# Optimization experiments

Hardware: AMD Instinct MI355X
Metric: run time of the kernel (lower is better)

Reference implementation:

```python
import jax, jax.numpy as jnp
import numpy as np

N_HEAD = 16
N_EMBD = 1024
B, T = 4, 2048


def setup_inputs() -> dict:
    key = jax.random.key(0)
    ks = jax.random.split(key, 5)
    s_in = 1.0 / np.sqrt(N_EMBD)
    return {
        "x": jax.random.normal(ks[0], (B, T, N_EMBD), dtype=jnp.float32),
        "W_qkv": jax.random.normal(ks[1], (N_EMBD, 3 * N_EMBD), dtype=jnp.float32) * s_in,
        "b_qkv": jnp.zeros((3 * N_EMBD,), dtype=jnp.float32),
        "W_proj": jax.random.normal(ks[2], (N_EMBD, N_EMBD), dtype=jnp.float32) * s_in,
        "b_proj": jnp.zeros((N_EMBD,), dtype=jnp.float32),
    }


def reference(x, W_qkv, b_qkv, W_proj, b_proj):
    Bb, Tt, C = x.shape
    H = N_HEAD
    hd = C // H  # head dim
    qkv = x @ W_qkv + b_qkv                      # [B,T,3C]
    q, k, v = jnp.split(qkv, 3, axis=-1)
    # [B,H,T,hd]
    q = q.reshape(Bb, Tt, H, hd).transpose(0, 2, 1, 3)
    k = k.reshape(Bb, Tt, H, hd).transpose(0, 2, 1, 3)
    v = v.reshape(Bb, Tt, H, hd).transpose(0, 2, 1, 3)
    scale = 1.0 / np.sqrt(hd).astype(np.float32)
    att = jnp.einsum("bhqd,bhkd->bhqk", q, k) * scale
    causal = jnp.tril(jnp.ones((Tt, Tt), dtype=bool))
    att = jnp.where(causal, att, jnp.float32(-jnp.inf))
    att = jax.nn.softmax(att, axis=-1)
    y = jnp.einsum("bhqk,bhkd->bhqd", att, v)    # [B,H,T,hd]
    y = y.transpose(0, 2, 1, 3).reshape(Bb, Tt, C)
    return y @ W_proj + b_proj
```

## Files before the change

kernel.cpp:

```cpp
#include <hip/hip_runtime.h>
#include <hip/hip_bf16.h>
#include <math.h>

typedef unsigned short u16;
typedef _Float16 f16_t;
typedef f16_t f16x8 __attribute__((ext_vector_type(8)));
typedef float f32x4 __attribute__((ext_vector_type(4)));

#define N_HEADC 16
#define C_EMBD  1024
#define B_SZ    4
#define T_SEQ   2048
#define HD      64
#define M_TOT   (B_SZ * T_SEQ)

#define BM 128
#define BN 256
#define BK 32
#define NT (C_EMBD / BK)
#define A_T (BM * BK)
#define B_T (BN * BK)

#define SWZ_CHUNK(l) ((((l) & 3) ^ (((l) >> 3) & 3)) * 8)

__device__ __forceinline__ u16 f2h(float f) {
    f16_t h = (f16_t)f;
    return __builtin_bit_cast(u16, h);
}
__device__ __forceinline__ unsigned pkf16(float a, float b) {
    unsigned lo = f2h(a), hi = f2h(b);
    return lo | (hi << 16);
}
__device__ __forceinline__ float fexp2(float x) {
#if __has_builtin(__builtin_amdgcn_exp2f)
    return __builtin_amdgcn_exp2f(x);
#else
    return exp2f(x);
#endif
}
__device__ __forceinline__ void gl_lds16(const u16* g, u16* l) {
    __builtin_amdgcn_global_load_lds(
        (const __attribute__((address_space(1))) unsigned int*)g,
        (__attribute__((address_space(3))) unsigned int*)l,
        16, 0, 0);
}

__global__ __launch_bounds__(256) void prep(const float* __restrict__ x,
                                            const float* __restrict__ Wqkv,
                                            const float* __restrict__ Wproj,
                                            u16* __restrict__ xh,
                                            u16* __restrict__ WqkvT,
                                            u16* __restrict__ WprojT) {
    __shared__ float tile[32][33];
    int bid = blockIdx.x, tid = threadIdx.x;
    if (bid < 8192) {
        int i = bid * 1024 + tid * 4;
        float4 v = *(const float4*)(x + i);
        ushort4 o;
        o.x = f2h(v.x); o.y = f2h(v.y); o.z = f2h(v.z); o.w = f2h(v.w);
        *(ushort4*)(xh + i) = o;
        return;
    }
    const float* in; u16* outp; int N, bx, by;
    if (bid < 8192 + 3072) {
        int b2 = bid - 8192; bx = b2 % 96; by = b2 / 96;
        in = Wqkv; outp = WqkvT; N = 3 * C_EMBD;
    } else {
        int b2 = bid - 11264; bx = b2 % 32; by = b2 / 32;
        in = Wproj; outp = WprojT; N = C_EMBD;
    }
    int tx = tid & 31, ty = tid >> 5;
    int n0 = bx * 32, k0 = by * 32;
    for (int i = ty; i < 32; i += 8)
        tile[i][tx] = in[(size_t)(k0 + i) * N + n0 + tx];
    __syncthreads();
    for (int i = ty; i < 32; i += 8)
        outp[(size_t)(n0 + i) * C_EMBD + k0 + tx] = f2h(tile[tx][i]);
}

__global__ __launch_bounds__(512) void gemm_qkv(const u16* __restrict__ A,
                                                const u16* __restrict__ BT,
                                                const float* __restrict__ bias,
                                                u16* __restrict__ qQ,
                                                u16* __restrict__ qK,
                                                u16* __restrict__ qVt) {
    __shared__ __align__(16) u16 smem[2 * A_T + 2 * B_T];
    u16* sA = smem;
    u16* sB = smem + 2 * A_T;
    int m0 = blockIdx.y * BM;
    int n0 = blockIdx.x * BN;
    int tid = threadIdx.x;
    int w = tid >> 6, lane = tid & 63;
    int wm = w >> 2, wn = w & 3;
    int quad = lane >> 4, rl = lane & 15;
    int srow = lane >> 2, sko = SWZ_CHUNK(lane);
    int kx = (rl >> 1) & 3;
    int qx = (quad ^ kx) * 8;

    f32x4 acc[4][4];
    #pragma unroll
    for (int i = 0; i < 4; ++i)
        #pragma unroll
        for (int j = 0; j < 4; ++j)
            acc[i][j] = f32x4{0.f, 0.f, 0.f, 0.f};

    const u16* gA  = A  + (size_t)(m0 + w * 16 + srow) * C_EMBD + sko;
    const u16* gB0 = BT + (size_t)(n0 + w * 16 + srow) * C_EMBD + sko;
    const u16* gB1 = gB0 + (size_t)128 * C_EMBD;

    gl_lds16(gA,  sA + w * 512);
    gl_lds16(gB0, sB + w * 512);
    gl_lds16(gB1, sB + 128 * BK + w * 512);
    gA += BK; gB0 += BK; gB1 += BK;

    for (int t = 0; t < NT; ++t) {
        asm volatile("s_waitcnt vmcnt(0)" ::: "memory");
        asm volatile("s_barrier" ::: "memory");
        const u16* pA = sA + (t & 1) * A_T + (wm * 64) * BK;
        const u16* pB = sB + (t & 1) * B_T + (wn * 64) * BK;
        f16x8 af[4], bfr[4];
        #pragma unroll
        for (int i = 0; i < 4; ++i)
            af[i] = *(const f16x8*)&pA[(i * 16 + rl) * BK + qx];
        bfr[0] = *(const f16x8*)&pB[(0 * 16 + rl) * BK + qx];
        bfr[1] = *(const f16x8*)&pB[(1 * 16 + rl) * BK + qx];
        if (t + 1 < NT) {
            int ns = (t + 1) & 1;
            gl_lds16(gA,  sA + ns * A_T + w * 512);
            gl_lds16(gB0, sB + ns * B_T + w * 512);
        }
        asm volatile("s_barrier" ::: "memory");
        __builtin_amdgcn_s_setprio(1);
        #pragma unroll
        for (int j = 0; j < 2; ++j)
            #pragma unroll
            for (int i = 0; i < 4; ++i)
                acc[i][j] = __builtin_amdgcn_mfma_f32_16x16x32_f16(
                    af[i], bfr[j], acc[i][j], 0, 0, 0);
        __builtin_amdgcn_s_setprio(0);
        asm volatile("s_barrier" ::: "memory");
        bfr[2] = *(const f16x8*)&pB[(2 * 16 + rl) * BK + qx];
        bfr[3] = *(const f16x8*)&pB[(3 * 16 + rl) * BK + qx];
        if (t + 1 < NT) {
            gl_lds16(gB1, sB + ((t + 1) & 1) * B_T + 128 * BK + w * 512);
            gA += BK; gB0 += BK; gB1 += BK;
        }
        asm volatile("s_barrier" ::: "memory");
        __builtin_amdgcn_s_setprio(1);
        #pragma unroll
        for (int j = 2; j < 4; ++j)
            #pragma unroll
            for (int i = 0; i < 4; ++i)
                acc[i][j] = __builtin_amdgcn_mfma_f32_16x16x32_f16(
                    af[i], bfr[j], acc[i][j], 0, 0, 0);
        __builtin_amdgcn_s_setprio(0);
    }

    __syncthreads();

    const float QSC = 0.18033688011112042f;
    int p = n0 >> 10;
    if (p < 2) {
        u16* ep = smem;
        u16* dst = p == 0 ? qQ : qK;
        float sc = p == 0 ? QSC : 1.0f;
        int hbase = (n0 & 1023) >> 6;
        #pragma unroll
        for (int c = 0; c < 4; ++c) {
            if (c) __syncthreads();
            if (wn == c) {
                #pragma unroll
                for (int j = 0; j < 4; ++j) {
                    float bv = bias[n0 + c * 64 + j * 16 + rl];
                    int col = (j * 16 + rl) ^ ((quad >> 1) << 4);
                    #pragma unroll
                    for (int i = 0; i < 4; ++i) {
                        int row = wm * 64 + i * 16 + quad * 4;
                        #pragma unroll
                        for (int r = 0; r < 4; ++r)
                            ep[(row + r) * 72 + col] = f2h((acc[i][j][r] + bv) * sc);
                    }
                }
            }
            __syncthreads();
            size_t rowbase = ((size_t)(m0 >> 11) * N_HEADC + hbase + c) * T_SEQ
                           + (m0 & 2047);
            #pragma unroll
            for (int s = 0; s < 2; ++s) {
                int task = s * 512 + tid;
                int row = task >> 3, seg = task & 7;
                int colr = (seg * 8) ^ (((row >> 3) & 1) << 4);
                *(uint4*)&dst[(rowbase + row) * HD + seg * 8] =
                    *(const uint4*)&ep[row * 72 + colr];
            }
        }
    } else {
        u16 (*tr)[136] = (u16 (*)[136])smem;
        int bb = m0 >> 11, t0g = m0 & 2047;
        #pragma unroll
        for (int c = 0; c < 4; ++c) {
            if (c) __syncthreads();
            if (wn == c) {
                #pragma unroll
                for (int j = 0; j < 4; ++j) {
                    int rowr = j * 16 + rl;
                    float bv = bias[n0 + c * 64 + rowr];
                    #pragma unroll
                    for (int i = 0; i < 4; ++i) {
                        int mm = wm * 64 + i * 16 + quad * 4;
                        *(unsigned*)&tr[rowr][mm]     = pkf16(acc[i][j][0] + bv, acc[i][j][1] + bv);
                        *(unsigned*)&tr[rowr][mm + 2] = pkf16(acc[i][j][2] + bv, acc[i][j][3] + bv);
                    }
                }
            }
            __syncthreads();
            #pragma unroll
            for (int s = 0; s < 2; ++s) {
                int task = s * 512 + tid;
                int nn = task >> 4, seg = task & 15;
                int ch = (n0 & 1023) + c * 64 + nn;
                int h = ch >> 6, d = ch & 63;
                size_t di = (((size_t)bb * N_HEADC + h) * HD + d) * T_SEQ + t0g + seg * 8;
                *(uint4*)&qVt[di] = *(const uint4*)&tr[nn][seg * 8];
            }
        }
    }
}

__global__ __launch_bounds__(512) void gemm_proj(const u16* __restrict__ A,
                                                 const u16* __restrict__ BT,
                                                 const float* __restrict__ bias,
                                                 float* __restrict__ out) {
    __shared__ __align__(16) u16 smem[3 * A_T + 3 * B_T];
    u16* sA = smem;
    u16* sB = smem + 3 * A_T;
    int m0 = blockIdx.y * BM;
    int n0 = blockIdx.x * BN;
    int tid = threadIdx.x;
    int w = tid >> 6, lane = tid & 63;
    int wm = w >> 2, wn = w & 3;
    int quad = lane >> 4, rl = lane & 15;
    int srow = lane >> 2, sko = SWZ_CHUNK(lane);
    int kx = (rl >> 1) & 3;
    int qx = (quad ^ kx) * 8;

    f32x4 acc[4][4];
    #pragma unroll
    for (int i = 0; i < 4; ++i)
        #pragma unroll
        for (int j = 0; j < 4; ++j)
            acc[i][j] = f32x4{0.f, 0.f, 0.f, 0.f};

    const u16* gA  = A  + (size_t)(m0 + w * 16 + srow) * C_EMBD + sko;
    const u16* gB0 = BT + (size_t)(n0 + w * 16 + srow) * C_EMBD + sko;
    const u16* gB1 = gB0 + (size_t)128 * C_EMBD;
    gl_lds16(gA,       sA + w * 512);
    gl_lds16(gB0,      sB + w * 512);
    gl_lds16(gB1,      sB + 128 * BK + w * 512);
    gl_lds16(gA + BK,  sA + A_T + w * 512);
    gl_lds16(gB0 + BK, sB + B_T + w * 512);
    gl_lds16(gB1 + BK, sB + B_T + 128 * BK + w * 512);
    gA += 2 * BK; gB0 += 2 * BK; gB1 += 2 * BK;
    int bufR = 0, bufS = 2;
    for (int t = 0; t < NT; ++t) {
        if (t == NT - 1) asm volatile("s_waitcnt vmcnt(0)" ::: "memory");
        else             asm volatile("s_waitcnt vmcnt(3)" ::: "memory");
        asm volatile("s_barrier" ::: "memory");
        const u16* pA = sA + bufR * A_T + (wm * 64) * BK;
        const u16* pB = sB + bufR * B_T + (wn * 64) * BK;
        f16x8 af[4], bfr[4];
        #pragma unroll
        for (int i = 0; i < 4; ++i)
            af[i] = *(const f16x8*)&pA[(i * 16 + rl) * BK + qx];
        bfr[0] = *(const f16x8*)&pB[(0 * 16 + rl) * BK + qx];
        bfr[1] = *(const f16x8*)&pB[(1 * 16 + rl) * BK + qx];
        if (t + 2 < NT) {
            gl_lds16(gA,  sA + bufS * A_T + w * 512);
            gl_lds16(gB0, sB + bufS * B_T + w * 512);
        }
        asm volatile("s_barrier" ::: "memory");
        __builtin_amdgcn_s_setprio(1);
        #pragma unroll
        for (int j = 0; j < 2; ++j)
            #pragma unroll
            for (int i = 0; i < 4; ++i)
                acc[i][j] = __builtin_amdgcn_mfma_f32_16x16x32_f16(
                    af[i], bfr[j], acc[i][j], 0, 0, 0);
        __builtin_amdgcn_s_setprio(0);
        asm volatile("s_barrier" ::: "memory");
        bfr[2] = *(const f16x8*)&pB[(2 * 16 + rl) * BK + qx];
        bfr[3] = *(const f16x8*)&pB[(3 * 16 + rl) * BK + qx];
        if (t + 2 < NT) {
            gl_lds16(gB1, sB + bufS * B_T + 128 * BK + w * 512);
            gA += BK; gB0 += BK; gB1 += BK;
        }
        asm volatile("s_barrier" ::: "memory");
        __builtin_amdgcn_s_setprio(1);
        #pragma unroll
        for (int j = 2; j < 4; ++j)
            #pragma unroll
            for (int i = 0; i < 4; ++i)
                acc[i][j] = __builtin_amdgcn_mfma_f32_16x16x32_f16(
                    af[i], bfr[j], acc[i][j], 0, 0, 0);
        __builtin_amdgcn_s_setprio(0);
        bufR = bufR == 2 ? 0 : bufR + 1;
        bufS = bufS == 2 ? 0 : bufS + 1;
    }

    #pragma unroll
    for (int i = 0; i < 4; ++i) {
        int mbase = m0 + wm * 64 + i * 16 + quad * 4;
        #pragma unroll
        for (int j = 0; j < 4; ++j) {
            int n = n0 + wn * 64 + j * 16 + rl;
            float bv = bias[n];
            #pragma unroll
            for (int r = 0; r < 4; ++r)
                out[(size_t)(mbase + r) * C_EMBD + n] = acc[i][j][r] + bv;
        }
    }
}

__global__ __launch_bounds__(512) void attn_mfma(const u16* __restrict__ Qg,
                                                 const u16* __restrict__ Kg,
                                                 const u16* __restrict__ Vtg,
                                                 u16* __restrict__ yh) {
    int bid = blockIdx.x;
    int a  = bid >> 6;
    int g  = bid & 63;
    int j  = a < 4 ? a : 11 - a;
    int h = g & 15, b = g >> 4;
    const size_t hs = (size_t)T_SEQ * HD;
    const u16* Qp  = Qg  + ((size_t)b * N_HEADC + h) * hs;
    const u16* Kp  = Kg  + ((size_t)b * N_HEADC + h) * hs;
    const u16* Vtp = Vtg + ((size_t)b * N_HEADC + h) * hs;

    __shared__ __align__(16) u16 sK[2][2][64][32];
    __shared__ __align__(16) u16 sVt[2][2][64][32];
    __shared__ __align__(16) u16 sP[8][32][72];

    int tid = threadIdx.x;
    int lane = tid & 63, w = tid >> 6;
    int quad = lane >> 4, rl = lane & 15;
    int kx = (rl >> 1) & 3;
    int qx = (quad ^ kx) * 8;
    u16* sPw = &sP[w][0][0];
    int srow = lane >> 2;
    int sch = SWZ_CHUNK(lane);
    const f32x4 mneg = {-4.f, -4.f, -4.f, -4.f};

    int qt  = (w < 4) ? (15 - j) : j;
    int q0w = qt * 128 + (w & 3) * 32;
    int nkt = 2 * (15 - j) + 2;

    const u16* gp[2];
    u16* ld0[2]; u16* ld1[2];
    int gstep;
    if (w < 4) {
        gstep = 64 * HD;
        int half = (w >> 1) & 1, rbase = (w & 1) * 32;
        #pragma unroll
        for (int c = 0; c < 2; ++c) {
            int r = rbase + c * 16;
            gp[c]  = Kp + (size_t)(r + srow) * HD + half * 32 + sch;
            ld0[c] = &sK[0][half][r][0];
            ld1[c] = &sK[1][half][r][0];
        }
    } else {
        gstep = 64;
        int v = w - 4;
        int half = (v >> 1) & 1, rbase = (v & 1) * 32;
        #pragma unroll
        for (int c = 0; c < 2; ++c) {
            int r = rbase + c * 16;
            gp[c]  = Vtp + (size_t)(r + srow) * T_SEQ + half * 32 + sch;
            ld0[c] = &sVt[0][half][r][0];
            ld1[c] = &sVt[1][half][r][0];
        }
    }

    f16x8 qf[2][2];
    #pragma unroll
    for (int nt = 0; nt < 2; ++nt)
        #pragma unroll
        for (int ks = 0; ks < 2; ++ks)
            qf[nt][ks] = *(const f16x8*)&Qp[(size_t)(q0w + nt * 16 + rl) * HD + ks * 32 + quad * 8];

    f32x4 O[2][4];
    #pragma unroll
    for (int mi = 0; mi < 2; ++mi)
        #pragma unroll
        for (int nd = 0; nd < 4; ++nd)
            O[mi][nd] = f32x4{0.f, 0.f, 0.f, 0.f};
    float l_[2] = {0.f, 0.f};

    gl_lds16(gp[0], ld0[0]);
    gl_lds16(gp[1], ld0[1]);

    for (int kt = 0; kt < nkt; ++kt) {
        __syncthreads();
        int buf = kt & 1;
        int k0 = kt * 64;
        if (kt + 1 < nkt) {
            u16* const* ldn = ((kt + 1) & 1) ? ld1 : ld0;
            #pragma unroll
            for (int c = 0; c < 2; ++c) {
                gp[c] += gstep;
                gl_lds16(gp[c], ldn[c]);
            }
        }
        if (k0 > q0w + 31) continue;

        f32x4 st[4][2];
        #pragma unroll
        for (int mt = 0; mt < 4; ++mt) {
            f16x8 ak0 = *(const f16x8*)&sK[buf][0][mt * 16 + rl][qx];
            f16x8 ak1 = *(const f16x8*)&sK[buf][1][mt * 16 + rl][qx];
            #pragma unroll
            for (int nt = 0; nt < 2; ++nt) {
                f32x4 t = __builtin_amdgcn_mfma_f32_16x16x32_f16(ak0, qf[nt][0], mneg, 0, 0, 0);
                st[mt][nt] = __builtin_amdgcn_mfma_f32_16x16x32_f16(ak1, qf[nt][1], t, 0, 0, 0);
            }
        }

        if (k0 + 63 > q0w) {
            #pragma unroll
            for (int mt = 0; mt < 4; ++mt)
                #pragma unroll
                for (int nt = 0; nt < 2; ++nt)
                    #pragma unroll
                    for (int r = 0; r < 4; ++r) {
                        int kpos = k0 + mt * 16 + quad * 4 + r;
                        int q = q0w + nt * 16 + rl;
                        if (kpos > q) st[mt][nt][r] = -INFINITY;
                    }
        }

        #pragma unroll
        for (int nt = 0; nt < 2; ++nt) {
            float lsum = 0.f;
            #pragma unroll
            for (int mt = 0; mt < 4; ++mt) {
                float p0 = fexp2(st[mt][nt][0]);
                float p1 = fexp2(st[mt][nt][1]);
                float p2 = fexp2(st[mt][nt][2]);
                float p3 = fexp2(st[mt][nt][3]);
                lsum += (p0 + p1) + (p2 + p3);
                *(uint2*)&sPw[(nt * 16 + rl) * 72 + mt * 16 + quad * 4] =
                    make_uint2(pkf16(p0, p1), pkf16(p2, p3));
            }
            l_[nt] += lsum;
        }

        #pragma unroll
        for (int ks = 0; ks < 2; ++ks) {
            f16x8 ap0 = *(const f16x8*)&sPw[(0 * 16 + rl) * 72 + ks * 32 + quad * 8];
            f16x8 ap1 = *(const f16x8*)&sPw[(1 * 16 + rl) * 72 + ks * 32 + quad * 8];
            #pragma unroll
            for (int nd = 0; nd < 4; ++nd) {
                f16x8 bv = *(const f16x8*)&sVt[buf][ks][nd * 16 + rl][qx];
                O[0][nd] = __builtin_amdgcn_mfma_f32_16x16x32_f16(ap0, bv, O[0][nd], 0, 0, 0);
                O[1][nd] = __builtin_amdgcn_mfma_f32_16x16x32_f16(ap1, bv, O[1][nd], 0, 0, 0);
            }
        }
    }

    #pragma unroll
    for (int nt = 0; nt < 2; ++nt) {
        l_[nt] += __shfl_xor(l_[nt], 16);
        l_[nt] += __shfl_xor(l_[nt], 32);
    }
    float linv[2] = {1.f / l_[0], 1.f / l_[1]};
    int idxq = quad * 4;
    #pragma unroll
    for (int mi = 0; mi < 2; ++mi)
        #pragma unroll
        for (int r = 0; r < 4; ++r) {
            float li = __shfl(linv[mi], idxq + r);
            int qg = q0w + mi * 16 + quad * 4 + r;
            size_t base = ((size_t)b * T_SEQ + qg) * C_EMBD + h * HD;
            #pragma unroll
            for (int nd = 0; nd < 4; ++nd)
                yh[base + nd * 16 + rl] = f2h(O[mi][nd][r] * li);
        }
}

extern "C" void kernel_launch(void* const* d_in, const int* in_sizes, int n_in,
                              void* d_out, int out_size, void* d_ws, size_t ws_size,
                              hipStream_t stream) {
    const float* x     = (const float*)d_in[0];
    const float* Wqkv  = (const float*)d_in[1];
    const float* bqkv  = (const float*)d_in[2];
    const float* Wproj = (const float*)d_in[3];
    const float* bproj = (const float*)d_in[4];
    float* out = (float*)d_out;

    char* ws = (char*)d_ws;
    u16* xh     = (u16*)(ws);
    u16* WqkvT  = (u16*)(ws + (size_t)16 * 1024 * 1024);
    u16* WprojT = (u16*)(ws + (size_t)22 * 1024 * 1024);
    u16* qQ     = (u16*)(ws + (size_t)24 * 1024 * 1024);
    u16* qK     = (u16*)(ws + (size_t)40 * 1024 * 1024);
    u16* qVt    = (u16*)(ws + (size_t)56 * 1024 * 1024);
    u16* yh     = (u16*)(ws + (size_t)72 * 1024 * 1024);

    prep<<<dim3(12288), dim3(256), 0, stream>>>(x, Wqkv, Wproj, xh, WqkvT, WprojT);
    gemm_qkv<<<dim3(3 * C_EMBD / BN, M_TOT / BM), dim3(512), 0, stream>>>(
        xh, WqkvT, bqkv, qQ, qK, qVt);
    attn_mfma<<<dim3(512), dim3(512), 0, stream>>>(
        qQ, qK, qVt, yh);
    gemm_proj<<<dim3(C_EMBD / BN, M_TOT / BM), dim3(512), 0, stream>>>(
        yh, WprojT, bproj, out);
}
```

Measured before the change: 237.3 us.

## Use 4-wave QKV GEMM with triple buffering and rework attention query tiling

The QKV GEMM drops to 256 threads, so each wave now computes a 128x64 tile. It switches from double to triple-buffered LDS with a partial vmcnt wait, so global loads overlap compute. The epilogue is now per-wave in private LDS regions, which removes the block-wide barriers between column chunks. The attention kernel changes its block-to-query-tile mapping from paired heavy/light 128-row tiles to single 256-row tiles ordered largest first. That trades causal load balancing within a block for simpler scheduling, and the larger per-wave accumulators raise register pressure.

```diff
diff --git a/kernel.cpp b/kernel.cpp
--- a/kernel.cpp
+++ b/kernel.cpp
@@ -20,6 +20,7 @@
 #define NT (C_EMBD / BK)
 #define A_T (BM * BK)
 #define B_T (BN * BK)
+#define SMEM_U16 (3 * A_T + 3 * B_T)
 
 #define SWZ_CHUNK(l) ((((l) & 3) ^ (((l) >> 3) & 3)) * 8)
 
@@ -78,151 +79,153 @@
         outp[(size_t)(n0 + i) * C_EMBD + k0 + tx] = f2h(tile[tx][i]);
 }
 
-__global__ __launch_bounds__(512) void gemm_qkv(const u16* __restrict__ A,
+__global__ __launch_bounds__(256) void gemm_qkv(const u16* __restrict__ A,
                                                 const u16* __restrict__ BT,
                                                 const float* __restrict__ bias,
                                                 u16* __restrict__ qQ,
                                                 u16* __restrict__ qK,
                                                 u16* __restrict__ qVt) {
-    __shared__ __align__(16) u16 smem[2 * A_T + 2 * B_T];
+    __shared__ __align__(16) u16 smem[SMEM_U16];
     u16* sA = smem;
-    u16* sB = smem + 2 * A_T;
+    u16* sB = smem + 3 * A_T;
     int m0 = blockIdx.y * BM;
     int n0 = blockIdx.x * BN;
     int tid = threadIdx.x;
     int w = tid >> 6, lane = tid & 63;
-    int wm = w >> 2, wn = w & 3;
     int quad = lane >> 4, rl = lane & 15;
     int srow = lane >> 2, sko = SWZ_CHUNK(lane);
     int kx = (rl >> 1) & 3;
     int qx = (quad ^ kx) * 8;
 
-    f32x4 acc[4][4];
-    #pragma unroll
-    for (int i = 0; i < 4; ++i)
+    f32x4 acc[8][4];
+    #pragma unroll
+    for (int i = 0; i < 8; ++i)
         #pragma unroll
         for (int j = 0; j < 4; ++j)
             acc[i][j] = f32x4{0.f, 0.f, 0.f, 0.f};
 
-    const u16* gA  = A  + (size_t)(m0 + w * 16 + srow) * C_EMBD + sko;
-    const u16* gB0 = BT + (size_t)(n0 + w * 16 + srow) * C_EMBD + sko;
-    const u16* gB1 = gB0 + (size_t)128 * C_EMBD;
-
-    gl_lds16(gA,  sA + w * 512);
-    gl_lds16(gB0, sB + w * 512);
-    gl_lds16(gB1, sB + 128 * BK + w * 512);
-    gA += BK; gB0 += BK; gB1 += BK;
-
+    const u16* gA0 = A + (size_t)(m0 + w * 32 + srow) * C_EMBD + sko;
+    const u16* gA1 = gA0 + 16 * C_EMBD;
+    const u16* gB0 = BT + (size_t)(n0 + w * 64 + srow) * C_EMBD + sko;
+    const u16* gB1 = gB0 + 16 * C_EMBD;
+    const u16* gB2 = gB0 + 32 * C_EMBD;
+    const u16* gB3 = gB0 + 48 * C_EMBD;
+
+    #pragma unroll
+    for (int s = 0; s < 2; ++s) {
+        int ko = s * BK;
+        gl_lds16(gA0 + ko, sA + s * A_T + (w * 32) * BK);
+        gl_lds16(gA1 + ko, sA + s * A_T + (w * 32 + 16) * BK);
+        gl_lds16(gB0 + ko, sB + s * B_T + (w * 64) * BK);
+        gl_lds16(gB1 + ko, sB + s * B_T + (w * 64 + 16) * BK);
+        gl_lds16(gB2 + ko, sB + s * B_T + (w * 64 + 32) * BK);
+        gl_lds16(gB3 + ko, sB + s * B_T + (w * 64 + 48) * BK);
+    }
+    gA0 += 2 * BK; gA1 += 2 * BK;
+    gB0 += 2 * BK; gB1 += 2 * BK; gB2 += 2 * BK; gB3 += 2 * BK;
+
+    int bufR = 0, bufS = 2;
     for (int t = 0; t < NT; ++t) {
-        asm volatile("s_waitcnt vmcnt(0)" ::: "memory");
-        asm volatile("s_barrier" ::: "memory");
-        const u16* pA = sA + (t & 1) * A_T + (wm * 64) * BK;
-        const u16* pB = sB + (t & 1) * B_T + (wn * 64) * BK;
-        f16x8 af[4], bfr[4];
-        #pragma unroll
-        for (int i = 0; i < 4; ++i)
+        if (t == NT - 1) asm volatile("s_waitcnt vmcnt(0)" ::: "memory");
+        else             asm volatile("s_waitcnt vmcnt(6)" ::: "memory");
+        asm volatile("s_barrier" ::: "memory");
+        const u16* pA = sA + bufR * A_T;
+        const u16* pB = sB + bufR * B_T + (w * 64) * BK;
+        f16x8 af[8], bfr[4];
+        #pragma unroll
+        for (int i = 0; i < 8; ++i)
             af[i] = *(const f16x8*)&pA[(i * 16 + rl) * BK + qx];
         bfr[0] = *(const f16x8*)&pB[(0 * 16 + rl) * BK + qx];
         bfr[1] = *(const f16x8*)&pB[(1 * 16 + rl) * BK + qx];
-        if (t + 1 < NT) {
-            int ns = (t + 1) & 1;
-            gl_lds16(gA,  sA + ns * A_T + w * 512);
-            gl_lds16(gB0, sB + ns * B_T + w * 512);
+        if (t + 2 < NT) {
+            gl_lds16(gA0, sA + bufS * A_T + (w * 32) * BK);
+            gl_lds16(gA1, sA + bufS * A_T + (w * 32 + 16) * BK);
+            gl_lds16(gB0, sB + bufS * B_T + (w * 64) * BK);
+            gl_lds16(gB1, sB + bufS * B_T + (w * 64 + 16) * BK);
         }
         asm volatile("s_barrier" ::: "memory");
         __builtin_amdgcn_s_setprio(1);
         #pragma unroll
         for (int j = 0; j < 2; ++j)
             #pragma unroll
-            for (int i = 0; i < 4; ++i)
+            for (int i = 0; i < 8; ++i)
                 acc[i][j] = __builtin_amdgcn_mfma_f32_16x16x32_f16(
                     af[i], bfr[j], acc[i][j], 0, 0, 0);
         __builtin_amdgcn_s_setprio(0);
         asm volatile("s_barrier" ::: "memory");
         bfr[2] = *(const f16x8*)&pB[(2 * 16 + rl) * BK + qx];
         bfr[3] = *(const f16x8*)&pB[(3 * 16 + rl) * BK + qx];
-        if (t + 1 < NT) {
-            gl_lds16(gB1, sB + ((t + 1) & 1) * B_T + 128 * BK + w * 512);
-            gA += BK; gB0 += BK; gB1 += BK;
+        if (t + 2 < NT) {
+            gl_lds16(gB2, sB + bufS * B_T + (w * 64 + 32) * BK);
+            gl_lds16(gB3, sB + bufS * B_T + (w * 64 + 48) * BK);
+            gA0 += BK; gA1 += BK;
+            gB0 += BK; gB1 += BK; gB2 += BK; gB3 += BK;
         }
         asm volatile("s_barrier" ::: "memory");
         __builtin_amdgcn_s_setprio(1);
         #pragma unroll
         for (int j = 2; j < 4; ++j)
             #pragma unroll
-            for (int i = 0; i < 4; ++i)
+            for (int i = 0; i < 8; ++i)
                 acc[i][j] = __builtin_amdgcn_mfma_f32_16x16x32_f16(
                     af[i], bfr[j], acc[i][j], 0, 0, 0);
         __builtin_amdgcn_s_setprio(0);
+        bufR = bufR == 2 ? 0 : bufR + 1;
+        bufS = bufS == 2 ? 0 : bufS + 1;
     }
 
     __syncthreads();
 
     const float QSC = 0.18033688011112042f;
     int p = n0 >> 10;
+    int hch = ((n0 & 1023) + w * 64) >> 6;
     if (p < 2) {
-        u16* ep = smem;
         u16* dst = p == 0 ? qQ : qK;
         float sc = p == 0 ? QSC : 1.0f;
-        int hbase = (n0 & 1023) >> 6;
-        #pragma unroll
-        for (int c = 0; c < 4; ++c) {
-            if (c) __syncthreads();
-            if (wn == c) {
+        u16* myep = smem + w * 9216;
+        #pragma unroll
+        for (int j = 0; j < 4; ++j) {
+            float bv = bias[n0 + w * 64 + j * 16 + rl];
+            int col = (j * 16 + rl) ^ ((quad >> 1) << 4);
+            #pragma unroll
+            for (int i = 0; i < 8; ++i) {
+                int row = i * 16 + quad * 4;
                 #pragma unroll
-                for (int j = 0; j < 4; ++j) {
-                    float bv = bias[n0 + c * 64 + j * 16 + rl];
-                    int col = (j * 16 + rl) ^ ((quad >> 1) << 4);
-                    #pragma unroll
-                    for (int i = 0; i < 4; ++i) {
-                        int row = wm * 64 + i * 16 + quad * 4;
-                        #pragma unroll
-                        for (int r = 0; r < 4; ++r)
-                            ep[(row + r) * 72 + col] = f2h((acc[i][j][r] + bv) * sc);
-                    }
-                }
+                for (int r = 0; r < 4; ++r)
+                    myep[(row + r) * 72 + col] = f2h((acc[i][j][r] + bv) * sc);
             }
-            __syncthreads();
-            size_t rowbase = ((size_t)(m0 >> 11) * N_HEADC + hbase + c) * T_SEQ
-                           + (m0 & 2047);
-            #pragma unroll
-            for (int s = 0; s < 2; ++s) {
-                int task = s * 512 + tid;
-                int row = task >> 3, seg = task & 7;
-                int colr = (seg * 8) ^ (((row >> 3) & 1) << 4);
-                *(uint4*)&dst[(rowbase + row) * HD + seg * 8] =
-                    *(const uint4*)&ep[row * 72 + colr];
+        }
+        size_t rowbase = ((size_t)(m0 >> 11) * N_HEADC + hch) * T_SEQ
+                       + (m0 & 2047);
+        #pragma unroll
+        for (int it = 0; it < 16; ++it) {
+            int idx = it * 64 + lane;
+            int row = idx >> 3, seg = idx & 7;
+            int col = (seg * 8) ^ (((row >> 3) & 1) << 4);
+            *(uint4*)&dst[(rowbase + row) * HD + seg * 8] =
+                *(const uint4*)&myep[row * 72 + col];
+        }
+    } else {
+        u16 (*tr)[136] = (u16 (*)[136])(smem + w * 9216);
+        int bb = m0 >> 11, t0g = m0 & 2047;
+        #pragma unroll
+        for (int j = 0; j < 4; ++j) {
+            int rowr = j * 16 + rl;
+            float bv = bias[n0 + w * 64 + rowr];
+            #pragma unroll
+            for (int i = 0; i < 8; ++i) {
+                int mm = i * 16 + quad * 4;
+                *(unsigned*)&tr[rowr][mm]     = pkf16(acc[i][j][0] + bv, acc[i][j][1] + bv);
+                *(unsigned*)&tr[rowr][mm + 2] = pkf16(acc[i][j][2] + bv, acc[i][j][3] + bv);
             }
         }
-    } else {
-        u16 (*tr)[136] = (u16 (*)[136])smem;
-        int bb = m0 >> 11, t0g = m0 & 2047;
-        #pragma unroll
-        for (int c = 0; c < 4; ++c) {
-            if (c) __syncthreads();
-            if (wn == c) {
-                #pragma unroll
-                for (int j = 0; j < 4; ++j) {
-                    int rowr = j * 16 + rl;
-                    float bv = bias[n0 + c * 64 + rowr];
-                    #pragma unroll
-                    for (int i = 0; i < 4; ++i) {
-                        int mm = wm * 64 + i * 16 + quad * 4;
-                        *(unsigned*)&tr[rowr][mm]     = pkf16(acc[i][j][0] + bv, acc[i][j][1] + bv);
-                        *(unsigned*)&tr[rowr][mm + 2] = pkf16(acc[i][j][2] + bv, acc[i][j][3] + bv);
-                    }
-                }
-            }
-            __syncthreads();
-            #pragma unroll
-            for (int s = 0; s < 2; ++s) {
-                int task = s * 512 + tid;
-                int nn = task >> 4, seg = task & 15;
-                int ch = (n0 & 1023) + c * 64 + nn;
-                int h = ch >> 6, d = ch & 63;
-                size_t di = (((size_t)bb * N_HEADC + h) * HD + d) * T_SEQ + t0g + seg * 8;
-                *(uint4*)&qVt[di] = *(const uint4*)&tr[nn][seg * 8];
-            }
+        size_t dbase = (((size_t)bb * N_HEADC + hch) * HD) * T_SEQ + t0g;
+        #pragma unroll
+        for (int it = 0; it < 16; ++it) {
+            int idx = it * 64 + lane;
+            int d = idx >> 4, seg = idx & 15;
+            *(uint4*)&qVt[dbase + (size_t)d * T_SEQ + seg * 8] =
+                *(const uint4*)&tr[d][seg * 8];
         }
     }
 }
@@ -231,7 +234,7 @@
                                                  const u16* __restrict__ BT,
                                                  const float* __restrict__ bias,
                                                  float* __restrict__ out) {
-    __shared__ __align__(16) u16 smem[3 * A_T + 3 * B_T];
+    __shared__ __align__(16) u16 smem[SMEM_U16];
     u16* sA = smem;
     u16* sB = smem + 3 * A_T;
     int m0 = blockIdx.y * BM;
@@ -254,12 +257,14 @@
     const u16* gA  = A  + (size_t)(m0 + w * 16 + srow) * C_EMBD + sko;
     const u16* gB0 = BT + (size_t)(n0 + w * 16 + srow) * C_EMBD + sko;
     const u16* gB1 = gB0 + (size_t)128 * C_EMBD;
-    gl_lds16(gA,       sA + w * 512);
-    gl_lds16(gB0,      sB + w * 512);
-    gl_lds16(gB1,      sB + 128 * BK + w * 512);
-    gl_lds16(gA + BK,  sA + A_T + w * 512);
-    gl_lds16(gB0 + BK, sB + B_T + w * 512);
-    gl_lds16(gB1 + BK, sB + B_T + 128 * BK + w * 512);
+    u16* lA = sA + w * 512;
+    u16* lB = sB + w * 512;
+    gl_lds16(gA,       lA);
+    gl_lds16(gB0,      lB);
+    gl_lds16(gB1,      lB + 128 * BK);
+    gl_lds16(gA + BK,  lA + A_T);
+    gl_lds16(gB0 + BK, lB + B_T);
+    gl_lds16(gB1 + BK, lB + B_T + 128 * BK);
     gA += 2 * BK; gB0 += 2 * BK; gB1 += 2 * BK;
     int bufR = 0, bufS = 2;
     for (int t = 0; t < NT; ++t) {
@@ -328,7 +333,7 @@
     int bid = blockIdx.x;
     int a  = bid >> 6;
     int g  = bid & 63;
-    int j  = a < 4 ? a : 11 - a;
+    int qt = a < 4 ? 7 - a : a - 4;
     int h = g & 15, b = g >> 4;
     const size_t hs = (size_t)T_SEQ * HD;
     const u16* Qp  = Qg  + ((size_t)b * N_HEADC + h) * hs;
@@ -349,9 +354,8 @@
     int sch = SWZ_CHUNK(lane);
     const f32x4 mneg = {-4.f, -4.f, -4.f, -4.f};
 
-    int qt  = (w < 4) ? (15 - j) : j;
-    int q0w = qt * 128 + (w & 3) * 32;
-    int nkt = 2 * (15 - j) + 2;
+    int q0w = qt * 256 + w * 32;
+    int nkt = 4 * (qt + 1);
 
     const u16* gp[2];
     u16* ld0[2]; u16* ld1[2];
@@ -505,7 +509,7 @@
     u16* yh     = (u16*)(ws + (size_t)72 * 1024 * 1024);
 
     prep<<<dim3(12288), dim3(256), 0, stream>>>(x, Wqkv, Wproj, xh, WqkvT, WprojT);
-    gemm_qkv<<<dim3(3 * C_EMBD / BN, M_TOT / BM), dim3(512), 0, stream>>>(
+    gemm_qkv<<<dim3(3 * C_EMBD / BN, M_TOT / BM), dim3(256), 0, stream>>>(
         xh, WqkvT, bqkv, qQ, qK, qVt);
     attn_mfma<<<dim3(512), dim3(512), 0, stream>>>(
         qQ, qK, qVt, yh);
```

Measured after the change: 267.3 us. +12.6%, slower.
